# Optimization experiments

Hardware: AMD Instinct MI355X
Metric: run time of the kernel (lower is better)

## Reference

```python
import jax, jax.numpy as jnp
import numpy as np

D_MODEL = 256

def setup_inputs() -> dict:
    key = jax.random.key(0)
    k1, k2, k3, k4, k5, k6 = jax.random.split(key, 6)
    B, LQ, LK, D = 16, 2048, 2048, D_MODEL
    q = jax.random.normal(k1, (B, LQ, D), dtype=jnp.float32)
    k = jax.random.normal(k2, (B, LK, D), dtype=jnp.float32)
    tsp = jax.random.normal(k3, (B, LK, D), dtype=jnp.float32)
    # xavier_uniform for w_qk [D, D] (no bias)
    bound = float(np.sqrt(6.0 / (D + D)))
    w_qk = jax.random.uniform(k4, (D, D), minval=-bound, maxval=bound, dtype=jnp.float32)
    # linear1: default torch init kaiming-uniform-ish; any values fine for correctness baseline
    lim = float(1.0 / np.sqrt(D))
    w1 = jax.random.uniform(k5, (D, D), minval=-lim, maxval=lim, dtype=jnp.float32)
    b1 = jax.random.uniform(k6, (D,), minval=-lim, maxval=lim, dtype=jnp.float32)
    return {"q": q, "k": k, "tsp": tsp, "w_qk": w_qk, "w1": w1, "b1": b1}

def reference(q, k, tsp, w_qk, w1, b1):
    d_head = q.shape[-1]
    temperature = jnp.asarray(np.power(d_head, 0.5), dtype=q.dtype)
    residual = q
    # shared Q/K projection (torch Linear: x @ W^T)
    qp = jnp.einsum('bqd,ed->bqe', q, w_qk)            # [B, Lq, Dh]
    kp = jnp.einsum('bkd,ed->bke', k, w_qk)            # [B, Lk, Dh]
    logits = jnp.einsum('bqd,bkd->bqk', qp, kp) / temperature  # [B, Lq, Lk]
    attn = jax.nn.softmax(logits, axis=2)
    # sigmoid is monotonic: max(sigmoid(x)) == sigmoid(max(x))
    prob_fg = jax.nn.sigmoid(jnp.max(logits, axis=-1, keepdims=True))  # [B, Lq, 1]
    out = jnp.einsum('bqk,bkd->bqd', attn, tsp)        # [B, Lq, Dh]
    gated = (residual + out) * prob_fg
    return jnp.einsum('bqd,ed->bqe', gated, w1) + b1
```

## Files before the change

kernel.cpp:

```cpp
#include <hip/hip_runtime.h>
#include <hip/hip_bf16.h>

typedef __bf16 bf16;
typedef __bf16 bf16x8 __attribute__((ext_vector_type(8)));
typedef __bf16 bf16x4 __attribute__((ext_vector_type(4)));
typedef __bf16 bf16x2 __attribute__((ext_vector_type(2)));
typedef float f32x4 __attribute__((ext_vector_type(4)));

static __device__ __forceinline__ f32x4 mfma16(bf16x8 a, bf16x8 b, f32x4 c) {
    return __builtin_amdgcn_mfma_f32_16x16x32_bf16(a, b, c, 0, 0, 0);
}

static __device__ __forceinline__ void load16_to_lds(const void* g, void* l) {
    __builtin_amdgcn_global_load_lds(
        (const __attribute__((address_space(1))) unsigned int*)g,
        (__attribute__((address_space(3))) unsigned int*)l, 16, 0, 0);
}

#define LKV 2048
#define DM 256

__global__ void convert_two(const float* __restrict__ a, bf16* __restrict__ da,
                            const float* __restrict__ b, bf16* __restrict__ db) {
    int blk = blockIdx.x;
    const float* src = (blk < 64) ? a : b;
    bf16* dst = (blk < 64) ? da : db;
    int i = (blk & 63) * 256 + threadIdx.x;
    float4 v = *(const float4*)(src + (size_t)i * 4);
    bf16x4 o;
    o[0] = (bf16)v.x; o[1] = (bf16)v.y; o[2] = (bf16)v.z; o[3] = (bf16)v.w;
    *(bf16x4*)(dst + (size_t)i * 4) = o;
}

__global__ __launch_bounds__(256) void transpose_tsp(const float* __restrict__ src,
                                                     bf16* __restrict__ dst) {
    __shared__ float tile[64][65];
    const int tid = threadIdx.x;
    const int b = blockIdx.z;
    const int kv0 = blockIdx.x * 64, d0 = blockIdx.y * 64;
#pragma unroll
    for (int i = 0; i < 4; ++i) {
        int idx = i * 256 + tid;
        int kv = idx >> 4, c4 = (idx & 15) * 4;
        float4 v = *(const float4*)(src + ((long)(b * LKV + kv0 + kv)) * DM + d0 + c4);
        tile[kv][c4 + 0] = v.x; tile[kv][c4 + 1] = v.y;
        tile[kv][c4 + 2] = v.z; tile[kv][c4 + 3] = v.w;
    }
    __syncthreads();
#pragma unroll
    for (int i = 0; i < 2; ++i) {
        int idx = i * 256 + tid;
        int d = idx >> 3, kc = idx & 7;
        bf16x8 o;
#pragma unroll
        for (int j = 0; j < 8; ++j) o[j] = (bf16)tile[kc * 8 + j][d];
        *(bf16x8*)(dst + ((long)(b * DM + d0 + d)) * LKV + kv0 + kc * 8) = o;
    }
}

template<bool IN_BF16, bool OUT_BF16, bool HAS_BIAS>
static __device__ __forceinline__ void gemm_body(const void* __restrict__ Xv,
                                                 const bf16* __restrict__ W,
                                                 const float* __restrict__ bias,
                                                 float scale, void* __restrict__ Y,
                                                 long rowbase) {
    __shared__ __align__(16) bf16 Xl[64][264];
    __shared__ __align__(16) bf16 Wl[256][40];
    const int tid  = threadIdx.x;
    const int lane = tid & 63, wave = tid >> 6;
    const int hi = lane >> 4, lo = lane & 15;

    if (IN_BF16) {
        const bf16* Xb = (const bf16*)Xv;
#pragma unroll
        for (int i = 0; i < 8; ++i) {
            int idx = i * 256 + tid;
            int r = idx >> 5, c8 = (idx & 31) * 8;
            uint4 v = *(const uint4*)(Xb + (rowbase + r) * 256 + c8);
            *(uint4*)(&Xl[r][c8]) = v;
        }
    } else {
        const float* X = (const float*)Xv;
#pragma unroll
        for (int i = 0; i < 16; ++i) {
            int idx4 = i * 256 + tid;
            int e = idx4 * 4;
            int r = e >> 8, c = e & 255;
            float4 v = *(const float4*)(X + (rowbase + r) * 256 + c);
            bf16x4 o;
            o[0] = (bf16)v.x; o[1] = (bf16)v.y; o[2] = (bf16)v.z; o[3] = (bf16)v.w;
            *(bf16x4*)(&Xl[r][c]) = o;
        }
    }

    f32x4 acc[16];
    const f32x4 zero = {0.f, 0.f, 0.f, 0.f};
#pragma unroll
    for (int n = 0; n < 16; ++n) acc[n] = zero;

    for (int ks = 0; ks < 8; ++ks) {
        __syncthreads();
#pragma unroll
        for (int c = 0; c < 4; ++c) {
            int idx = c * 256 + tid;
            int e = idx >> 2, part = idx & 3;
            uint4 v = *(const uint4*)((const char*)W + (size_t)e * 512 + ks * 64 + part * 16);
            *(uint4*)((char*)&Wl[0][0] + e * 80 + part * 16) = v;
        }
        __syncthreads();
        bf16x8 a = *(const bf16x8*)((const char*)&Xl[0][0] + (wave * 16 + lo) * 528 + ks * 64 + hi * 16);
#pragma unroll
        for (int n = 0; n < 16; ++n) {
            bf16x8 bfr = *(const bf16x8*)((const char*)&Wl[0][0] + (n * 16 + lo) * 80 + hi * 16);
            acc[n] = mfma16(a, bfr, acc[n]);
        }
    }

#pragma unroll
    for (int n = 0; n < 16; ++n) {
        int col = n * 16 + lo;
        float bv = HAS_BIAS ? bias[col] : 0.f;
#pragma unroll
        for (int r = 0; r < 4; ++r) {
            long row = rowbase + wave * 16 + hi * 4 + r;
            float v = acc[n][r] * scale + bv;
            if (OUT_BF16) ((bf16*)Y)[row * 256 + col] = (bf16)v;
            else          ((float*)Y)[row * 256 + col] = v;
        }
    }
}

__global__ __launch_bounds__(256) void gemm_qk(const float* __restrict__ q,
                                               const float* __restrict__ k,
                                               const bf16* __restrict__ W,
                                               bf16* __restrict__ qp,
                                               bf16* __restrict__ kp) {
    bool is_k = blockIdx.x >= 512;
    const float* X = is_k ? k : q;
    bf16* Y = is_k ? kp : qp;
    float scale = is_k ? 1.0f : 0.0625f;
    long rowbase = (long)(blockIdx.x & 511) * 64;
    gemm_body<false, true, false>(X, W, nullptr, scale, Y, rowbase);
}

__global__ __launch_bounds__(256) void gemm_out(const bf16* __restrict__ gated,
                                                const bf16* __restrict__ W,
                                                const float* __restrict__ bias,
                                                float* __restrict__ out) {
    gemm_body<true, false, true>(gated, W, bias, 1.0f, out, (long)blockIdx.x * 64);
}

__global__ __launch_bounds__(256, 2) void flash4(const bf16* __restrict__ qp,
                                                 const bf16* __restrict__ kp,
                                                 const bf16* __restrict__ tspT,
                                                 const float* __restrict__ qorig,
                                                 bf16* __restrict__ gated) {
    __shared__ __align__(16) char kp_lds[2][32 * 512];
    __shared__ __align__(16) char tsp_lds[2][256 * 64];
    const int tid  = threadIdx.x;
    const int lane = tid & 63, wave = tid >> 6;
    const int hi = lane >> 4, lo = lane & 15;

    int id  = (int)blockIdx.x;
    int bid = (id & 7) * 64 + (id >> 3);
    const int b  = bid >> 5;
    const int qb = bid & 31;
    const long qbase = (long)b * LKV + qb * 64;
    const char* kp_g  = (const char*)(kp + (long)b * LKV * DM);
    const char* tsp_g = (const char*)(tspT + (long)b * DM * LKV);

    int kp_off[4], tsp_off[4];
#pragma unroll
    for (int j = 0; j < 4; ++j) {
        int kv = wave * 8 + j * 2 + (lane >> 5);
        kp_off[j] = kv * 512 + (((lane & 31) ^ (kv & 7)) << 4);
        int d = wave * 64 + j * 16 + (lane >> 2);
        int cp = (lane & 3) ^ ((lane >> 3) & 3);
        tsp_off[j] = d * 4096 + cp * 16;
    }

    int bp_src[4];
#pragma unroll
    for (int k2 = 0; k2 < 4; ++k2)
        bp_src[k2] = ((((hi & 1) * 2 + (k2 >> 1)) << 4) + lo) << 2;

    bf16x8 aq[8];
    {
        const bf16* qrow = qp + (qbase + wave * 16 + lo) * DM;
#pragma unroll
        for (int ks = 0; ks < 8; ++ks) aq[ks] = *(const bf16x8*)(qrow + ks * 32 + hi * 8);
    }

    bf16x8 ones;
#pragma unroll
    for (int j = 0; j < 8; ++j) ones[j] = (bf16)1.0f;

    f32x4 o[16], o_l;
    const f32x4 zero = {0.f, 0.f, 0.f, 0.f};
#pragma unroll
    for (int n = 0; n < 16; ++n) o[n] = zero;
    o_l = zero;
    float m = -1e30f, tm = -1e30f;

    const int kswz = (lo & 7) << 4;
    const int tswz = ((lo >> 1) & 3) << 4;

#pragma unroll
    for (int j = 0; j < 4; ++j) {
        load16_to_lds(kp_g + kp_off[j],  &kp_lds[0][wave * 4096 + j * 1024]);
        load16_to_lds(tsp_g + tsp_off[j], &tsp_lds[0][wave * 4096 + j * 1024]);
    }
    __syncthreads();

    for (int t = 0; t < 64; ++t) {
        const int cur = t & 1;
        if (t < 63) {
            const long ko = (long)(t + 1);
#pragma unroll
            for (int j = 0; j < 4; ++j) {
                load16_to_lds(kp_g + ko * 16384 + kp_off[j],  &kp_lds[cur ^ 1][wave * 4096 + j * 1024]);
                load16_to_lds(tsp_g + ko * 64 + tsp_off[j],   &tsp_lds[cur ^ 1][wave * 4096 + j * 1024]);
            }
        }

        f32x4 s[2];
        __builtin_amdgcn_s_setprio(1);
#pragma unroll
        for (int n = 0; n < 2; ++n) {
            s[n] = zero;
            const char* rowp = &kp_lds[cur][(n * 16 + lo) << 9];
#pragma unroll
            for (int ks = 0; ks < 8; ++ks) {
                bf16x8 kk = *(const bf16x8*)(rowp + ((ks * 64 + hi * 16) ^ kswz));
                s[n] = mfma16(kk, aq[ks], s[n]);
            }
        }
        __builtin_amdgcn_s_setprio(0);

        float pm = fmaxf(fmaxf(fmaxf(s[0][0], s[0][1]), fmaxf(s[0][2], s[0][3])),
                         fmaxf(fmaxf(s[1][0], s[1][1]), fmaxf(s[1][2], s[1][3])));
        pm = fmaxf(pm, __shfl_xor(pm, 16));
        pm = fmaxf(pm, __shfl_xor(pm, 32));
        tm = fmaxf(tm, pm);
        if (__any(pm > m + 8.f)) {
            float nm = fmaxf(m, pm);
            float a = __expf(m - nm);
            m = nm;
            o_l *= a;
#pragma unroll
            for (int n = 0; n < 16; ++n) o[n] *= a;
        }

        int cvt[2][2];
#pragma unroll
        for (int n = 0; n < 2; ++n)
#pragma unroll
            for (int c = 0; c < 2; ++c) {
                bf16x2 pr;
                pr[0] = (bf16)__expf(s[n][2 * c]     - m);
                pr[1] = (bf16)__expf(s[n][2 * c + 1] - m);
                cvt[n][c] = __builtin_bit_cast(int, pr);
            }
        int pki[4];
#pragma unroll
        for (int k2 = 0; k2 < 4; ++k2) {
            int a0 = __builtin_amdgcn_ds_bpermute(bp_src[k2], cvt[0][k2 & 1]);
            int a1 = __builtin_amdgcn_ds_bpermute(bp_src[k2], cvt[1][k2 & 1]);
            pki[k2] = (hi < 2) ? a0 : a1;
        }
        int4 pii = make_int4(pki[0], pki[1], pki[2], pki[3]);
        bf16x8 pk = __builtin_bit_cast(bf16x8, pii);

        o_l = mfma16(ones, pk, o_l);
        __builtin_amdgcn_s_setprio(1);
#pragma unroll
        for (int dt = 0; dt < 16; ++dt) {
            int d = dt * 16 + lo;
            bf16x8 tt = *(const bf16x8*)(&tsp_lds[cur][d * 64 + ((hi * 16) ^ tswz)]);
            o[dt] = mfma16(tt, pk, o[dt]);
        }
        __builtin_amdgcn_s_setprio(0);

        __syncthreads();
    }

    float prob = 1.f / (1.f + __expf(-tm));
    float invl = 1.f / o_l[0];
    long row = qbase + wave * 16 + lo;
#pragma unroll
    for (int dt = 0; dt < 16; ++dt) {
        int c0 = dt * 16 + hi * 4;
        float4 qv = *(const float4*)(qorig + row * 256 + c0);
        bf16x4 g;
        g[0] = (bf16)((qv.x + o[dt][0] * invl) * prob);
        g[1] = (bf16)((qv.y + o[dt][1] * invl) * prob);
        g[2] = (bf16)((qv.z + o[dt][2] * invl) * prob);
        g[3] = (bf16)((qv.w + o[dt][3] * invl) * prob);
        *(bf16x4*)(gated + row * 256 + c0) = g;
    }
}

extern "C" void kernel_launch(void* const* d_in, const int* in_sizes, int n_in,
                              void* d_out, int out_size, void* d_ws, size_t ws_size,
                              hipStream_t stream) {
    const float* q    = (const float*)d_in[0];
    const float* k    = (const float*)d_in[1];
    const float* tsp  = (const float*)d_in[2];
    const float* w_qk = (const float*)d_in[3];
    const float* w1   = (const float*)d_in[4];
    const float* b1   = (const float*)d_in[5];
    float* out = (float*)d_out;
    char* ws = (char*)d_ws;

    bf16* qp_b  = (bf16*)(ws + 0);
    bf16* kp_b  = (bf16*)(ws + 16777216);
    bf16* tspT  = (bf16*)(ws + 33554432);
    bf16* gated = (bf16*)(ws + 50331648);
    bf16* wqkb  = (bf16*)(ws + 67108864);
    bf16* w1b   = (bf16*)(ws + 67239936);

    convert_two<<<128, 256, 0, stream>>>(w_qk, wqkb, w1, w1b);

    dim3 tg(32, 4, 16);
    transpose_tsp<<<tg, 256, 0, stream>>>(tsp, tspT);

    gemm_qk<<<1024, 256, 0, stream>>>(q, k, wqkb, qp_b, kp_b);

    flash4<<<512, 256, 0, stream>>>(qp_b, kp_b, tspT, q, gated);

    gemm_out<<<512, 256, 0, stream>>>(gated, w1b, b1, out);
}
```

Baseline: 182.9 us.

## Software-pipeline flash loop with deeper prefetch and merge prep kernels

The attention loop is restructured so that the P·V MFMAs for tile t-1 are issued alongside the QK^T MFMAs for tile t. Prefetch now runs two tiles ahead, with a triple-buffered tsp LDS buffer and explicit vmcnt waits and s_barriers in place of __syncthreads. The intent is to overlap the softmax, exp and bpermute latency with matrix work and to hide global-to-LDS loads better. Separately, the weight conversion and tsp transpose kernels are merged into one launch to save a kernel launch. The cost is more LDS per block, which could reduce occupancy, and a more fragile synchronisation scheme.

```diff
diff --git a/kernel.cpp b/kernel.cpp
--- a/kernel.cpp
+++ b/kernel.cpp
@@ -20,29 +20,30 @@
 #define LKV 2048
 #define DM 256
 
-__global__ void convert_two(const float* __restrict__ a, bf16* __restrict__ da,
-                            const float* __restrict__ b, bf16* __restrict__ db) {
-    int blk = blockIdx.x;
-    const float* src = (blk < 64) ? a : b;
-    bf16* dst = (blk < 64) ? da : db;
-    int i = (blk & 63) * 256 + threadIdx.x;
-    float4 v = *(const float4*)(src + (size_t)i * 4);
-    bf16x4 o;
-    o[0] = (bf16)v.x; o[1] = (bf16)v.y; o[2] = (bf16)v.z; o[3] = (bf16)v.w;
-    *(bf16x4*)(dst + (size_t)i * 4) = o;
-}
-
-__global__ __launch_bounds__(256) void transpose_tsp(const float* __restrict__ src,
-                                                     bf16* __restrict__ dst) {
+__global__ __launch_bounds__(256) void prep(const float* __restrict__ wqk, bf16* __restrict__ wqkb,
+                                            const float* __restrict__ w1,  bf16* __restrict__ w1b,
+                                            const float* __restrict__ tsp, bf16* __restrict__ tspT) {
     __shared__ float tile[64][65];
     const int tid = threadIdx.x;
-    const int b = blockIdx.z;
-    const int kv0 = blockIdx.x * 64, d0 = blockIdx.y * 64;
+    int bid = (int)blockIdx.x;
+    if (bid < 128) {
+        const float* src = (bid < 64) ? wqk : w1;
+        bf16* dst = (bid < 64) ? wqkb : w1b;
+        int i = (bid & 63) * 256 + tid;
+        float4 v = *(const float4*)(src + (size_t)i * 4);
+        bf16x4 o;
+        o[0] = (bf16)v.x; o[1] = (bf16)v.y; o[2] = (bf16)v.z; o[3] = (bf16)v.w;
+        *(bf16x4*)(dst + (size_t)i * 4) = o;
+        return;
+    }
+    int id = bid - 128;
+    const int b = id >> 7;
+    const int kv0 = (id & 31) * 64, d0 = ((id >> 5) & 3) * 64;
 #pragma unroll
     for (int i = 0; i < 4; ++i) {
         int idx = i * 256 + tid;
         int kv = idx >> 4, c4 = (idx & 15) * 4;
-        float4 v = *(const float4*)(src + ((long)(b * LKV + kv0 + kv)) * DM + d0 + c4);
+        float4 v = *(const float4*)(tsp + ((long)(b * LKV + kv0 + kv)) * DM + d0 + c4);
         tile[kv][c4 + 0] = v.x; tile[kv][c4 + 1] = v.y;
         tile[kv][c4 + 2] = v.z; tile[kv][c4 + 3] = v.w;
     }
@@ -54,7 +55,7 @@
         bf16x8 o;
 #pragma unroll
         for (int j = 0; j < 8; ++j) o[j] = (bf16)tile[kc * 8 + j][d];
-        *(bf16x8*)(dst + ((long)(b * DM + d0 + d)) * LKV + kv0 + kc * 8) = o;
+        *(bf16x8*)(tspT + ((long)(b * DM + d0 + d)) * LKV + kv0 + kc * 8) = o;
     }
 }
 
@@ -150,13 +151,13 @@
     gemm_body<true, false, true>(gated, W, bias, 1.0f, out, (long)blockIdx.x * 64);
 }
 
-__global__ __launch_bounds__(256, 2) void flash4(const bf16* __restrict__ qp,
+__global__ __launch_bounds__(256, 2) void flash5(const bf16* __restrict__ qp,
                                                  const bf16* __restrict__ kp,
                                                  const bf16* __restrict__ tspT,
                                                  const float* __restrict__ qorig,
                                                  bf16* __restrict__ gated) {
-    __shared__ __align__(16) char kp_lds[2][32 * 512];
-    __shared__ __align__(16) char tsp_lds[2][256 * 64];
+    __shared__ __align__(16) char kbuf[2][16384];
+    __shared__ __align__(16) char tbuf[3][16384];
     const int tid  = threadIdx.x;
     const int lane = tid & 63, wave = tid >> 6;
     const int hi = lane >> 4, lo = lane & 15;
@@ -201,38 +202,53 @@
     for (int n = 0; n < 16; ++n) o[n] = zero;
     o_l = zero;
     float m = -1e30f, tm = -1e30f;
+    bf16x8 pk;
+#pragma unroll
+    for (int j = 0; j < 8; ++j) pk[j] = (bf16)0.0f;
 
     const int kswz = (lo & 7) << 4;
     const int tswz = ((lo >> 1) & 3) << 4;
 
 #pragma unroll
     for (int j = 0; j < 4; ++j) {
-        load16_to_lds(kp_g + kp_off[j],  &kp_lds[0][wave * 4096 + j * 1024]);
-        load16_to_lds(tsp_g + tsp_off[j], &tsp_lds[0][wave * 4096 + j * 1024]);
-    }
-    __syncthreads();
-
+        load16_to_lds(kp_g + kp_off[j],          &kbuf[0][wave * 4096 + j * 1024]);
+        load16_to_lds(tsp_g + tsp_off[j],        &tbuf[0][wave * 4096 + j * 1024]);
+    }
+#pragma unroll
+    for (int j = 0; j < 4; ++j) {
+        load16_to_lds(kp_g + 16384 + kp_off[j],  &kbuf[1][wave * 4096 + j * 1024]);
+        load16_to_lds(tsp_g + 64 + tsp_off[j],   &tbuf[1][wave * 4096 + j * 1024]);
+    }
+
+    int ts3 = 2;
     for (int t = 0; t < 64; ++t) {
-        const int cur = t & 1;
-        if (t < 63) {
-            const long ko = (long)(t + 1);
-#pragma unroll
-            for (int j = 0; j < 4; ++j) {
-                load16_to_lds(kp_g + ko * 16384 + kp_off[j],  &kp_lds[cur ^ 1][wave * 4096 + j * 1024]);
-                load16_to_lds(tsp_g + ko * 64 + tsp_off[j],   &tsp_lds[cur ^ 1][wave * 4096 + j * 1024]);
-            }
-        }
+        if (t < 63) { asm volatile("s_waitcnt vmcnt(8)" ::: "memory"); }
+        else        { asm volatile("s_waitcnt vmcnt(0)" ::: "memory"); }
+        __builtin_amdgcn_sched_barrier(0);
+        __builtin_amdgcn_s_barrier();
+        __builtin_amdgcn_sched_barrier(0);
 
         f32x4 s[2];
+        const char* kb = kbuf[t & 1];
         __builtin_amdgcn_s_setprio(1);
 #pragma unroll
         for (int n = 0; n < 2; ++n) {
             s[n] = zero;
-            const char* rowp = &kp_lds[cur][(n * 16 + lo) << 9];
+            const char* rowp = kb + ((n * 16 + lo) << 9);
 #pragma unroll
             for (int ks = 0; ks < 8; ++ks) {
                 bf16x8 kk = *(const bf16x8*)(rowp + ((ks * 64 + hi * 16) ^ kswz));
                 s[n] = mfma16(kk, aq[ks], s[n]);
+            }
+        }
+        if (t > 0) {
+            const char* tb = tbuf[ts3];
+            o_l = mfma16(ones, pk, o_l);
+#pragma unroll
+            for (int dt = 0; dt < 16; ++dt) {
+                int d = dt * 16 + lo;
+                bf16x8 tt = *(const bf16x8*)(tb + d * 64 + ((hi * 16) ^ tswz));
+                o[dt] = mfma16(tt, pk, o[dt]);
             }
         }
         __builtin_amdgcn_s_setprio(0);
@@ -250,7 +266,6 @@
 #pragma unroll
             for (int n = 0; n < 16; ++n) o[n] *= a;
         }
-
         int cvt[2][2];
 #pragma unroll
         for (int n = 0; n < 2; ++n)
@@ -269,19 +284,32 @@
             pki[k2] = (hi < 2) ? a0 : a1;
         }
         int4 pii = make_int4(pki[0], pki[1], pki[2], pki[3]);
-        bf16x8 pk = __builtin_bit_cast(bf16x8, pii);
-
+        pk = __builtin_bit_cast(bf16x8, pii);
+
+        __builtin_amdgcn_sched_barrier(0);
+        __builtin_amdgcn_s_barrier();
+        __builtin_amdgcn_sched_barrier(0);
+
+        if (t < 62) {
+            const long tile = (long)(t + 2);
+#pragma unroll
+            for (int j = 0; j < 4; ++j) {
+                load16_to_lds(kp_g + tile * 16384 + kp_off[j], &kbuf[t & 1][wave * 4096 + j * 1024]);
+                load16_to_lds(tsp_g + tile * 64 + tsp_off[j],  &tbuf[ts3][wave * 4096 + j * 1024]);
+            }
+        }
+        ts3 = (ts3 == 2) ? 0 : ts3 + 1;
+    }
+
+    {
+        const char* tb = tbuf[ts3];
         o_l = mfma16(ones, pk, o_l);
-        __builtin_amdgcn_s_setprio(1);
 #pragma unroll
         for (int dt = 0; dt < 16; ++dt) {
             int d = dt * 16 + lo;
-            bf16x8 tt = *(const bf16x8*)(&tsp_lds[cur][d * 64 + ((hi * 16) ^ tswz)]);
+            bf16x8 tt = *(const bf16x8*)(tb + d * 64 + ((hi * 16) ^ tswz));
             o[dt] = mfma16(tt, pk, o[dt]);
         }
-        __builtin_amdgcn_s_setprio(0);
-
-        __syncthreads();
     }
 
     float prob = 1.f / (1.f + __expf(-tm));
@@ -319,14 +347,11 @@
     bf16* wqkb  = (bf16*)(ws + 67108864);
     bf16* w1b   = (bf16*)(ws + 67239936);
 
-    convert_two<<<128, 256, 0, stream>>>(w_qk, wqkb, w1, w1b);
-
-    dim3 tg(32, 4, 16);
-    transpose_tsp<<<tg, 256, 0, stream>>>(tsp, tspT);
+    prep<<<2176, 256, 0, stream>>>(w_qk, wqkb, w1, w1b, tsp, tspT);
 
     gemm_qk<<<1024, 256, 0, stream>>>(q, k, wqkb, qp_b, kp_b);
 
-    flash4<<<512, 256, 0, stream>>>(qp_b, kp_b, tspT, q, gated);
+    flash5<<<512, 256, 0, stream>>>(qp_b, kp_b, tspT, q, gated);
 
     gemm_out<<<512, 256, 0, stream>>>(gated, w1b, b1, out);
 }
```

New measurement: 168.6 us. 1.08x faster.

## Fuse prep kernels, pre-swizzle tsp into MFMA fragment layout, triple-buffer K

Applied to the files above, without the earlier changes.

Merges the weight conversion, tsp transpose and Q/K projection into one prep launch. Weights are now converted from fp32 inside each GEMM's staging loop. tsp is written in a per-lane MFMA fragment layout so the flash kernel loads it straight into registers instead of going through LDS. K tiles use a three-slot LDS ring with explicit vmcnt waits and one barrier per iteration instead of two. This cuts launch count, LDS traffic and synchronisation. In exchange the weight conversion is repeated in every GEMM block and register pressure in the attention loop goes up.

```diff
diff --git a/kernel.cpp b/kernel.cpp
--- a/kernel.cpp
+++ b/kernel.cpp
@@ -20,52 +20,15 @@
 #define LKV 2048
 #define DM 256
 
-__global__ void convert_two(const float* __restrict__ a, bf16* __restrict__ da,
-                            const float* __restrict__ b, bf16* __restrict__ db) {
-    int blk = blockIdx.x;
-    const float* src = (blk < 64) ? a : b;
-    bf16* dst = (blk < 64) ? da : db;
-    int i = (blk & 63) * 256 + threadIdx.x;
-    float4 v = *(const float4*)(src + (size_t)i * 4);
-    bf16x4 o;
-    o[0] = (bf16)v.x; o[1] = (bf16)v.y; o[2] = (bf16)v.z; o[3] = (bf16)v.w;
-    *(bf16x4*)(dst + (size_t)i * 4) = o;
-}
-
-__global__ __launch_bounds__(256) void transpose_tsp(const float* __restrict__ src,
-                                                     bf16* __restrict__ dst) {
-    __shared__ float tile[64][65];
-    const int tid = threadIdx.x;
-    const int b = blockIdx.z;
-    const int kv0 = blockIdx.x * 64, d0 = blockIdx.y * 64;
-#pragma unroll
-    for (int i = 0; i < 4; ++i) {
-        int idx = i * 256 + tid;
-        int kv = idx >> 4, c4 = (idx & 15) * 4;
-        float4 v = *(const float4*)(src + ((long)(b * LKV + kv0 + kv)) * DM + d0 + c4);
-        tile[kv][c4 + 0] = v.x; tile[kv][c4 + 1] = v.y;
-        tile[kv][c4 + 2] = v.z; tile[kv][c4 + 3] = v.w;
-    }
-    __syncthreads();
-#pragma unroll
-    for (int i = 0; i < 2; ++i) {
-        int idx = i * 256 + tid;
-        int d = idx >> 3, kc = idx & 7;
-        bf16x8 o;
-#pragma unroll
-        for (int j = 0; j < 8; ++j) o[j] = (bf16)tile[kc * 8 + j][d];
-        *(bf16x8*)(dst + ((long)(b * DM + d0 + d)) * LKV + kv0 + kc * 8) = o;
-    }
-}
-
 template<bool IN_BF16, bool OUT_BF16, bool HAS_BIAS>
-static __device__ __forceinline__ void gemm_body(const void* __restrict__ Xv,
-                                                 const bf16* __restrict__ W,
+static __device__ __forceinline__ void gemm_body(char* smem,
+                                                 const void* __restrict__ Xv,
+                                                 const float* __restrict__ Wf,
                                                  const float* __restrict__ bias,
                                                  float scale, void* __restrict__ Y,
                                                  long rowbase) {
-    __shared__ __align__(16) bf16 Xl[64][264];
-    __shared__ __align__(16) bf16 Wl[256][40];
+    bf16* Xl  = (bf16*)smem;
+    char* WlB = smem + 33792;
     const int tid  = threadIdx.x;
     const int lane = tid & 63, wave = tid >> 6;
     const int hi = lane >> 4, lo = lane & 15;
@@ -77,7 +40,7 @@
             int idx = i * 256 + tid;
             int r = idx >> 5, c8 = (idx & 31) * 8;
             uint4 v = *(const uint4*)(Xb + (rowbase + r) * 256 + c8);
-            *(uint4*)(&Xl[r][c8]) = v;
+            *(uint4*)(Xl + r * 264 + c8) = v;
         }
     } else {
         const float* X = (const float*)Xv;
@@ -89,7 +52,7 @@
             float4 v = *(const float4*)(X + (rowbase + r) * 256 + c);
             bf16x4 o;
             o[0] = (bf16)v.x; o[1] = (bf16)v.y; o[2] = (bf16)v.z; o[3] = (bf16)v.w;
-            *(bf16x4*)(&Xl[r][c]) = o;
+            *(bf16x4*)(Xl + r * 264 + c) = o;
         }
     }
 
@@ -101,17 +64,19 @@
     for (int ks = 0; ks < 8; ++ks) {
         __syncthreads();
 #pragma unroll
-        for (int c = 0; c < 4; ++c) {
+        for (int c = 0; c < 8; ++c) {
             int idx = c * 256 + tid;
-            int e = idx >> 2, part = idx & 3;
-            uint4 v = *(const uint4*)((const char*)W + (size_t)e * 512 + ks * 64 + part * 16);
-            *(uint4*)((char*)&Wl[0][0] + e * 80 + part * 16) = v;
+            int e = idx >> 3, q4 = (idx & 7) * 4;
+            float4 v = *(const float4*)(Wf + e * 256 + ks * 32 + q4);
+            bf16x4 o;
+            o[0] = (bf16)v.x; o[1] = (bf16)v.y; o[2] = (bf16)v.z; o[3] = (bf16)v.w;
+            *(bf16x4*)(WlB + e * 80 + q4 * 2) = o;
         }
         __syncthreads();
-        bf16x8 a = *(const bf16x8*)((const char*)&Xl[0][0] + (wave * 16 + lo) * 528 + ks * 64 + hi * 16);
+        bf16x8 a = *(const bf16x8*)((const char*)Xl + (wave * 16 + lo) * 528 + ks * 64 + hi * 16);
 #pragma unroll
         for (int n = 0; n < 16; ++n) {
-            bf16x8 bfr = *(const bf16x8*)((const char*)&Wl[0][0] + (n * 16 + lo) * 80 + hi * 16);
+            bf16x8 bfr = *(const bf16x8*)(WlB + (n * 16 + lo) * 80 + hi * 16);
             acc[n] = mfma16(a, bfr, acc[n]);
         }
     }
@@ -130,33 +95,67 @@
     }
 }
 
-__global__ __launch_bounds__(256) void gemm_qk(const float* __restrict__ q,
+__global__ __launch_bounds__(256) void prep_qk(const float* __restrict__ q,
                                                const float* __restrict__ k,
-                                               const bf16* __restrict__ W,
+                                               const float* __restrict__ wqk,
+                                               const float* __restrict__ tsp,
                                                bf16* __restrict__ qp,
-                                               bf16* __restrict__ kp) {
-    bool is_k = blockIdx.x >= 512;
-    const float* X = is_k ? k : q;
-    bf16* Y = is_k ? kp : qp;
-    float scale = is_k ? 1.0f : 0.0625f;
-    long rowbase = (long)(blockIdx.x & 511) * 64;
-    gemm_body<false, true, false>(X, W, nullptr, scale, Y, rowbase);
+                                               bf16* __restrict__ kp,
+                                               bf16* __restrict__ tspF) {
+    __shared__ __align__(16) char smem[54272];
+    const int tid = threadIdx.x;
+    int bid = (int)blockIdx.x;
+    if (bid < 1024) {
+        bool is_k = bid >= 512;
+        gemm_body<false, true, false>(smem, is_k ? k : q, wqk, nullptr,
+                                      is_k ? 1.0f : 0.0625f, is_k ? kp : qp,
+                                      (long)(bid & 511) * 64);
+        return;
+    }
+    int id = bid - 1024;
+    const int b = id >> 7;
+    const int kv0 = (id & 31) * 64, d0 = ((id >> 5) & 3) * 64;
+    float (*tile)[65] = (float(*)[65])smem;
+#pragma unroll
+    for (int i = 0; i < 4; ++i) {
+        int idx = i * 256 + tid;
+        int kv = idx >> 4, c4 = (idx & 15) * 4;
+        float4 v = *(const float4*)(tsp + ((long)(b * LKV + kv0 + kv)) * DM + d0 + c4);
+        tile[kv][c4 + 0] = v.x; tile[kv][c4 + 1] = v.y;
+        tile[kv][c4 + 2] = v.z; tile[kv][c4 + 3] = v.w;
+    }
+    __syncthreads();
+    char* outb = (char*)tspF + ((long)b << 20);
+#pragma unroll
+    for (int i = 0; i < 2; ++i) {
+        int w = i * 256 + tid;
+        int ti = w >> 8;
+        int dti = (w >> 6) & 3;
+        int lane = w & 63;
+        int hi = lane >> 4, lo = lane & 15;
+        bf16x8 o;
+#pragma unroll
+        for (int j = 0; j < 8; ++j) o[j] = (bf16)tile[ti * 32 + hi * 8 + j][dti * 16 + lo];
+        int t_abs = (kv0 >> 5) + ti;
+        int dt_abs = (d0 >> 4) + dti;
+        *(bf16x8*)(outb + (((t_abs * 16 + dt_abs) << 6) + lane) * 16) = o;
+    }
 }
 
 __global__ __launch_bounds__(256) void gemm_out(const bf16* __restrict__ gated,
-                                                const bf16* __restrict__ W,
-                                                const float* __restrict__ bias,
+                                                const float* __restrict__ w1,
+                                                const float* __restrict__ b1,
                                                 float* __restrict__ out) {
-    gemm_body<true, false, true>(gated, W, bias, 1.0f, out, (long)blockIdx.x * 64);
-}
-
-__global__ __launch_bounds__(256, 2) void flash4(const bf16* __restrict__ qp,
+    __shared__ __align__(16) char smem[54272];
+    gemm_body<true, false, true>(smem, gated, w1, b1, 1.0f, out, (long)blockIdx.x * 64);
+}
+
+__global__ __launch_bounds__(256, 2) void flash6(const bf16* __restrict__ qp,
                                                  const bf16* __restrict__ kp,
-                                                 const bf16* __restrict__ tspT,
+                                                 const bf16* __restrict__ tspF,
                                                  const float* __restrict__ qorig,
                                                  bf16* __restrict__ gated) {
-    __shared__ __align__(16) char kp_lds[2][32 * 512];
-    __shared__ __align__(16) char tsp_lds[2][256 * 64];
+    __shared__ __align__(16) char kbuf[3][16384];
     const int tid  = threadIdx.x;
     const int lane = tid & 63, wave = tid >> 6;
     const int hi = lane >> 4, lo = lane & 15;
@@ -167,16 +166,13 @@
     const int qb = bid & 31;
     const long qbase = (long)b * LKV + qb * 64;
     const char* kp_g  = (const char*)(kp + (long)b * LKV * DM);
-    const char* tsp_g = (const char*)(tspT + (long)b * DM * LKV);
-
-    int kp_off[4], tsp_off[4];
+    const char* tsp_f = (const char*)tspF + ((long)b << 20) + lane * 16;
+
+    int kp_off[4];
 #pragma unroll
     for (int j = 0; j < 4; ++j) {
         int kv = wave * 8 + j * 2 + (lane >> 5);
         kp_off[j] = kv * 512 + (((lane & 31) ^ (kv & 7)) << 4);
-        int d = wave * 64 + j * 16 + (lane >> 2);
-        int cp = (lane & 3) ^ ((lane >> 3) & 3);
-        tsp_off[j] = d * 4096 + cp * 16;
     }
 
     int bp_src[4];
@@ -203,32 +199,45 @@
     float m = -1e30f, tm = -1e30f;
 
     const int kswz = (lo & 7) << 4;
-    const int tswz = ((lo >> 1) & 3) << 4;
-
-#pragma unroll
-    for (int j = 0; j < 4; ++j) {
-        load16_to_lds(kp_g + kp_off[j],  &kp_lds[0][wave * 4096 + j * 1024]);
-        load16_to_lds(tsp_g + tsp_off[j], &tsp_lds[0][wave * 4096 + j * 1024]);
-    }
-    __syncthreads();
+
+#pragma unroll
+    for (int j = 0; j < 4; ++j)
+        load16_to_lds(kp_g + kp_off[j],          &kbuf[0][wave * 4096 + j * 1024]);
+#pragma unroll
+    for (int j = 0; j < 4; ++j)
+        load16_to_lds(kp_g + 16384 + kp_off[j],  &kbuf[1][wave * 4096 + j * 1024]);
 
     for (int t = 0; t < 64; ++t) {
-        const int cur = t & 1;
-        if (t < 63) {
-            const long ko = (long)(t + 1);
-#pragma unroll
-            for (int j = 0; j < 4; ++j) {
-                load16_to_lds(kp_g + ko * 16384 + kp_off[j],  &kp_lds[cur ^ 1][wave * 4096 + j * 1024]);
-                load16_to_lds(tsp_g + ko * 64 + tsp_off[j],   &tsp_lds[cur ^ 1][wave * 4096 + j * 1024]);
-            }
-        }
+        if (t == 0)       { asm volatile("s_waitcnt vmcnt(4)"  ::: "memory"); }
+        else if (t == 63) { asm volatile("s_waitcnt vmcnt(16)" ::: "memory"); }
+        else              { asm volatile("s_waitcnt vmcnt(20)" ::: "memory"); }
+        __builtin_amdgcn_sched_barrier(0);
+        __builtin_amdgcn_s_barrier();
+        __builtin_amdgcn_sched_barrier(0);
+
+        bf16x8 tt[16];
+        {
+            const char* tb = tsp_f + (long)t * 16384;
+#pragma unroll
+            for (int dt = 0; dt < 16; ++dt)
+                tt[dt] = *(const bf16x8*)(tb + dt * 1024);
+        }
+        if (t < 62) {
+            const int dslot = (t + 2) % 3;
+            const char* src = kp_g + (long)(t + 2) * 16384;
+#pragma unroll
+            for (int j = 0; j < 4; ++j)
+                load16_to_lds(src + kp_off[j], &kbuf[dslot][wave * 4096 + j * 1024]);
+        }
+        __builtin_amdgcn_sched_barrier(0);
 
         f32x4 s[2];
+        const char* kb = kbuf[t % 3];
         __builtin_amdgcn_s_setprio(1);
 #pragma unroll
         for (int n = 0; n < 2; ++n) {
             s[n] = zero;
-            const char* rowp = &kp_lds[cur][(n * 16 + lo) << 9];
+            const char* rowp = kb + ((n * 16 + lo) << 9);
 #pragma unroll
             for (int ks = 0; ks < 8; ++ks) {
                 bf16x8 kk = *(const bf16x8*)(rowp + ((ks * 64 + hi * 16) ^ kswz));
@@ -250,7 +259,6 @@
 #pragma unroll
             for (int n = 0; n < 16; ++n) o[n] *= a;
         }
-
         int cvt[2][2];
 #pragma unroll
         for (int n = 0; n < 2; ++n)
@@ -274,14 +282,9 @@
         o_l = mfma16(ones, pk, o_l);
         __builtin_amdgcn_s_setprio(1);
 #pragma unroll
-        for (int dt = 0; dt < 16; ++dt) {
-            int d = dt * 16 + lo;
-            bf16x8 tt = *(const bf16x8*)(&tsp_lds[cur][d * 64 + ((hi * 16) ^ tswz)]);
-            o[dt] = mfma16(tt, pk, o[dt]);
-        }
+        for (int dt = 0; dt < 16; ++dt)
+            o[dt] = mfma16(tt[dt], pk, o[dt]);
         __builtin_amdgcn_s_setprio(0);
-
-        __syncthreads();
     }
 
     float prob = 1.f / (1.f + __expf(-tm));
@@ -314,19 +317,12 @@
 
     bf16* qp_b  = (bf16*)(ws + 0);
     bf16* kp_b  = (bf16*)(ws + 16777216);
-    bf16* tspT  = (bf16*)(ws + 33554432);
+    bf16* tspF  = (bf16*)(ws + 33554432);
     bf16* gated = (bf16*)(ws + 50331648);
-    bf16* wqkb  = (bf16*)(ws + 67108864);
-    bf16* w1b   = (bf16*)(ws + 67239936);
-
-    convert_two<<<128, 256, 0, stream>>>(w_qk, wqkb, w1, w1b);
-
-    dim3 tg(32, 4, 16);
-    transpose_tsp<<<tg, 256, 0, stream>>>(tsp, tspT);
-
-    gemm_qk<<<1024, 256, 0, stream>>>(q, k, wqkb, qp_b, kp_b);
-
-    flash4<<<512, 256, 0, stream>>>(qp_b, kp_b, tspT, q, gated);
-
-    gemm_out<<<512, 256, 0, stream>>>(gated, w1b, b1, out);
-}
+
+    prep_qk<<<3072, 256, 0, stream>>>(q, k, w_qk, tsp, qp_b, kp_b, tspF);
+
+    flash6<<<512, 256, 0, stream>>>(qp_b, kp_b, tspF, q, gated);
+
+    gemm_out<<<512, 256, 0, stream>>>(gated, w1, b1, out);
+}
```

Result: no change. 182.4 us (-0.3%).
